# Performance work log

Hardware: AMD Instinct MI355X
Metric: run time of the kernel (lower is better)

Reference implementation:

```python
import jax, jax.numpy as jnp
import numpy as np

B, S, E, H, D, P = 4, 2048, 1024, 16, 64, 64  # batch, seq, embed, heads, head_dim, position_dim
MASKED_BIAS = -10000.0


def setup_inputs() -> dict:
    key = jax.random.key(0)
    ks = jax.random.split(key, 24)
    n = lambda k, sh: jax.random.normal(k, sh, dtype=jnp.float32)
    eyeD = jnp.eye(D, dtype=jnp.float32)
    eyeH = jnp.eye(H, dtype=jnp.float32)
    inp = {
        'hidden_states': n(ks[0], (B, S, E)),
        'position_states': n(ks[1], (B, S, P)),
        # Conv2D per-head projections (identity init + perturbation): [H, D, D]
        'Wq': eyeD[None] + 0.02 * n(ks[2], (H, D, D)), 'bq': 0.01 * n(ks[3], (H, D)),
        'Wk': eyeD[None] + 0.02 * n(ks[4], (H, D, D)), 'bk': 0.01 * n(ks[5], (H, D)),
        'Wv': eyeD[None] + 0.02 * n(ks[6], (H, D, D)), 'bv': 0.01 * n(ks[7], (H, D)),
        # Conv2D(transpose=True) cross-head mix: weight [H_out, H_in, D], bias [H, D]
        'Wqh': eyeH[:, :, None] + 0.02 * n(ks[8], (H, H, D)), 'bqh': 0.01 * n(ks[9], (H, D)),
        'Wkh': eyeH[:, :, None] + 0.02 * n(ks[10], (H, H, D)), 'bkh': 0.01 * n(ks[11], (H, D)),
        'Wvh': eyeH[:, :, None] + 0.02 * n(ks[12], (H, H, D)), 'bvh': 0.01 * n(ks[13], (H, D)),
        # p_attn Conv1D: position_dim -> 3*head_dim
        'Wp': 0.02 * n(ks[14], (P, 3 * D)), 'bp': 0.01 * n(ks[15], (3 * D,)),
        # position_conv expand: weight [3, 1, H], bias [H]
        'Wpe': 0.02 * n(ks[16], (3, 1, H)), 'bpe': 0.01 * n(ks[17], (H,)),
        # c_proj Conv1D: E -> E
        'Wc': 0.02 * n(ks[18], (E, E)), 'bc': 0.01 * n(ks[19], (E,)),
    }
    return inp


def _attention(hidden_states, position_states, Wq, bq, Wqh, bqh, Wk, bk, Wkh, bkh,
               Wv, bv, Wvh, bvh, Wp, bp, Wpe, bpe, Wc, bc):
    b, s, _ = hidden_states.shape
    x = hidden_states.reshape(b, s, H, D)

    def proj(Wa, ba, Wh, bh):
        # Conv2D: per-head linear within head_dim
        y = jnp.einsum('bshd,hde->bshe', x, Wa) + ba
        # Conv2D(transpose): mix across heads, per feature dim d
        return jnp.einsum('bshd,ghd->bsgd', y, Wh) + bh

    q = proj(Wq, bq, Wqh, bqh)  # [b,s,H,D]
    k = proj(Wk, bk, Wkh, bkh)
    v = proj(Wv, bv, Wvh, bvh)

    # p_attn (Conv1D) -> [b,s,3,D]; p_expand broadcasts each var across heads
    p = (position_states @ Wp + bp).reshape(b, s, 3, D)
    pe = p[..., None, :] * Wpe[:, 0, :][:, :, None] + bpe[:, None]  # [b,s,3,H,D]
    q = q + pe[:, :, 0]
    k = k + pe[:, :, 1]
    v = v + pe[:, :, 2]

    q = q.transpose(0, 2, 1, 3)  # [b,H,s,D]
    k = k.transpose(0, 2, 1, 3)
    v = v.transpose(0, 2, 1, 3)

    scores = jnp.einsum('bhqd,bhkd->bhqk', q, k) / jnp.sqrt(jnp.float32(D))
    causal = jnp.tril(jnp.ones((s, s), dtype=bool))
    scores = jnp.where(causal, scores, jnp.float32(MASKED_BIAS))
    w = jax.nn.softmax(scores, axis=-1)
    o = jnp.einsum('bhqk,bhkd->bhqd', w, v)
    o = o.transpose(0, 2, 1, 3).reshape(b, s, E)
    return o @ Wc + bc


def reference(hidden_states, position_states, Wq, bq, Wqh, bqh, Wk, bk, Wkh, bkh,
              Wv, bv, Wvh, bvh, Wp, bp, Wpe, bpe, Wc, bc):
    return _attention(hidden_states, position_states, Wq, bq, Wqh, bqh, Wk, bk,
                      Wkh, bkh, Wv, bv, Wvh, bvh, Wp, bp, Wpe, bpe, Wc, bc)
```

## Files before the change

kernel.cpp:

```cpp
#include <hip/hip_runtime.h>
#include <stdint.h>
#include <stddef.h>

using bf16x8 = __attribute__((ext_vector_type(8))) __bf16;
using f32x4  = __attribute__((ext_vector_type(4))) float;
using u16x8  = __attribute__((ext_vector_type(8))) unsigned short;
using u16x4  = __attribute__((ext_vector_type(4))) unsigned short;
typedef unsigned short u16;

#define DEV __device__ __forceinline__

#define QSCALE 0.18033688011112042f
#define SBIAS 32.0f

DEV u16 f2bf(float f) {
  unsigned u = __float_as_uint(f);
  u += 0x7fffu + ((u >> 16) & 1u);
  return (u16)(u >> 16);
}

DEV void gld_lds16(const u16* g, u16* l) {
  __builtin_amdgcn_global_load_lds(
      (__attribute__((address_space(1))) void*)g,
      (__attribute__((address_space(3))) void*)l, 16, 0, 0);
}

__global__ __launch_bounds__(256) void k_packA(const float* __restrict__ hs,
                                               const float* __restrict__ ps,
                                               u16* __restrict__ A) {
  int idx = blockIdx.x * 256 + threadIdx.x;
  int t  = idx / 272;
  int c4 = (idx - t * 272) * 4;
  float4 f;
  if (c4 < 1024) f = *(const float4*)(hs + (size_t)t * 1024 + c4);
  else           f = *(const float4*)(ps + (size_t)t * 64 + (c4 - 1024));
  u16x4 o4;
  o4[0] = f2bf(f.x); o4[1] = f2bf(f.y); o4[2] = f2bf(f.z); o4[3] = f2bf(f.w);
  *(u16x4*)(A + (size_t)t * 1088 + c4) = o4;
}

__global__ __launch_bounds__(256) void k_buildW(const float* __restrict__ Wq, const float* __restrict__ Wk,
                                                const float* __restrict__ Wv, const float* __restrict__ Wqh,
                                                const float* __restrict__ Wkh, const float* __restrict__ Wvh,
                                                const float* __restrict__ Wp, const float* __restrict__ Wpe,
                                                u16* __restrict__ Wt) {
  int idx = blockIdx.x * 256 + threadIdx.x;
  int n = idx / 1088, kk = idx - n * 1088;
  int which = n >> 10, g = (n >> 6) & 15, e = n & 63;
  const float* Wa = (which == 0) ? Wq : (which == 1) ? Wk : Wv;
  const float* Wh = (which == 0) ? Wqh : (which == 1) ? Wkh : Wvh;
  float val;
  if (kk < 1024) {
    int h = kk >> 6, d = kk & 63;
    val = Wa[(size_t)(h * 64 + d) * 64 + e] * Wh[(size_t)(g * 16 + h) * 64 + e];
  } else {
    int p = kk - 1024;
    val = Wp[(size_t)p * 192 + which * 64 + e] * Wpe[which * 16 + g];
  }
  if (which == 0) val *= QSCALE;
  Wt[idx] = f2bf(val);
}

__global__ __launch_bounds__(256) void k_buildBias(const float* __restrict__ bq, const float* __restrict__ bk,
                                                   const float* __restrict__ bv, const float* __restrict__ Wqh,
                                                   const float* __restrict__ Wkh, const float* __restrict__ Wvh,
                                                   const float* __restrict__ bqh, const float* __restrict__ bkh,
                                                   const float* __restrict__ bvh, const float* __restrict__ bp,
                                                   const float* __restrict__ Wpe, const float* __restrict__ bpe,
                                                   float* __restrict__ bias) {
  int n = blockIdx.x * 256 + threadIdx.x;
  int which = n >> 10, g = (n >> 6) & 15, e = n & 63;
  const float* ba = (which == 0) ? bq : (which == 1) ? bk : bv;
  const float* Wh = (which == 0) ? Wqh : (which == 1) ? Wkh : Wvh;
  const float* bh = (which == 0) ? bqh : (which == 1) ? bkh : bvh;
  float s = bh[g * 64 + e] + bp[which * 64 + e] * Wpe[which * 16 + g] + bpe[g];
  for (int h = 0; h < 16; ++h) s += ba[h * 64 + e] * Wh[(g * 16 + h) * 64 + e];
  if (which == 0) s *= QSCALE;
  bias[n] = s;
}

__global__ __launch_bounds__(256) void k_transWc(const float* __restrict__ Wc, u16* __restrict__ WcT) {
  __shared__ float tile[32][33];
  int tx = threadIdx.x & 31, ty = threadIdx.x >> 5;
  int n0 = blockIdx.x * 32, k0 = blockIdx.y * 32;
#pragma unroll
  for (int i = 0; i < 32; i += 8)
    tile[ty + i][tx] = Wc[(size_t)(k0 + ty + i) * 1024 + n0 + tx];
  __syncthreads();
#pragma unroll
  for (int i = 0; i < 32; i += 8)
    WcT[(size_t)(n0 + ty + i) * 1024 + k0 + tx] = f2bf(tile[tx][ty + i]);
}

template <int EPI>
__global__ __launch_bounds__(256) void gemm128(const u16* __restrict__ A, const u16* __restrict__ Bt,
                                               const float* __restrict__ bias,
                                               u16* __restrict__ qo, u16* __restrict__ ko, u16* __restrict__ vo,
                                               float* __restrict__ outf, int M, int N, int K, int NT) {
  __shared__ alignas(16) u16 As[2][8192];
  __shared__ alignas(16) u16 Bs[2][8192];
  const int tid = threadIdx.x;
  const int l = tid & 63, w = tid >> 6;
  const int lr = l & 15, lg = l >> 4;
  const int wm = w >> 1, wn = w & 1;

  const int nwg = gridDim.x;
  const int cpx = nwg >> 3;
  const int virt = (blockIdx.x & 7) * cpx + (blockIdx.x >> 3);
  const int m0 = (virt / NT) * 128, n0 = (virt - (virt / NT) * NT) * 128;

  const int KT = K >> 6;

  f32x4 acc[4][4] = {};

#pragma unroll
  for (int call = 0; call < 4; ++call) {
    int ci = (call * 4 + w) * 64 + l;
    int row = ci >> 3, s = ci & 7;
    int kq = (s ^ (row & 7)) * 8;
    gld_lds16(A + (size_t)(m0 + row) * K + kq, &As[0][(call * 4 + w) * 512]);
    gld_lds16(Bt + (size_t)(n0 + row) * K + kq, &Bs[0][(call * 4 + w) * 512]);
  }

  int cur = 0;
  for (int kt = 0; kt < KT; ++kt) {
    if (kt + 1 < KT) {
      const int kb = (kt + 1) * 64;
#pragma unroll
      for (int call = 0; call < 4; ++call) {
        int ci = (call * 4 + w) * 64 + l;
        int row = ci >> 3, s = ci & 7;
        int kq = (s ^ (row & 7)) * 8;
        gld_lds16(A + (size_t)(m0 + row) * K + kb + kq, &As[cur ^ 1][(call * 4 + w) * 512]);
        gld_lds16(Bt + (size_t)(n0 + row) * K + kb + kq, &Bs[cur ^ 1][(call * 4 + w) * 512]);
      }
      asm volatile("s_waitcnt vmcnt(8)" ::: "memory");
    } else {
      asm volatile("s_waitcnt vmcnt(0)" ::: "memory");
    }
    __builtin_amdgcn_s_barrier();
    asm volatile("" ::: "memory");

    const u16* AsC = As[cur];
    const u16* BsC = Bs[cur];
#pragma unroll
    for (int kk = 0; kk < 2; ++kk) {
      bf16x8 af[4], bfr[4];
#pragma unroll
      for (int mf = 0; mf < 4; ++mf) {
        int row = wm * 64 + mf * 16 + lr;
        int byo = row * 128 + (((kk * 32 + lg * 8) * 2) ^ ((row & 7) << 4));
        af[mf] = *(const bf16x8*)((const char*)AsC + byo);
      }
#pragma unroll
      for (int nf = 0; nf < 4; ++nf) {
        int row = wn * 64 + nf * 16 + lr;
        int byo = row * 128 + (((kk * 32 + lg * 8) * 2) ^ ((row & 7) << 4));
        bfr[nf] = *(const bf16x8*)((const char*)BsC + byo);
      }
      __builtin_amdgcn_s_setprio(1);
#pragma unroll
      for (int mf = 0; mf < 4; ++mf)
#pragma unroll
        for (int nf = 0; nf < 4; ++nf)
          acc[mf][nf] = __builtin_amdgcn_mfma_f32_16x16x32_bf16(af[mf], bfr[nf], acc[mf][nf], 0, 0, 0);
      __builtin_amdgcn_s_setprio(0);
    }

    asm volatile("s_waitcnt lgkmcnt(0)" ::: "memory");
    __builtin_amdgcn_s_barrier();
    asm volatile("" ::: "memory");
    cur ^= 1;
  }

#pragma unroll
  for (int mf = 0; mf < 4; ++mf)
#pragma unroll
    for (int nf = 0; nf < 4; ++nf)
#pragma unroll
      for (int r = 0; r < 4; ++r) {
        int row = m0 + wm * 64 + mf * 16 + lg * 4 + r;
        int col = n0 + wn * 64 + nf * 16 + lr;
        float val = acc[mf][nf][r] + bias[col];
        if (EPI == 0) {
          int which = col >> 10, g = (col >> 6) & 15, e = col & 63;
          int b = row >> 11, si = row & 2047;
          size_t idx = ((size_t)((b * 16 + g) * 2048 + si)) * 64 + e;
          u16 bvv = f2bf(val);
          if (which == 0) qo[idx] = bvv;
          else if (which == 1) ko[idx] = bvv;
          else vo[idx] = bvv;
        } else {
          outf[(size_t)row * N + col] = val;
        }
      }
}

__global__ __launch_bounds__(256) void k_transV(const u16* __restrict__ v, u16* __restrict__ vT) {
  __shared__ u16 t[64][65];
  int bh = blockIdx.y, s0 = blockIdx.x * 64;
  const u16* src = v + ((size_t)bh * 2048 + s0) * 64;
  u16* dst = vT + (size_t)bh * 64 * 2048 + s0;
  int tid = threadIdx.x;
#pragma unroll
  for (int it = 0; it < 2; ++it) {
    int ci = it * 256 + tid;
    int row = ci >> 3, sl = ci & 7;
    u16x8 val = *(const u16x8*)(src + (size_t)row * 64 + sl * 8);
#pragma unroll
    for (int jj = 0; jj < 8; ++jj) t[row][sl * 8 + jj] = val[jj];
  }
  __syncthreads();
#pragma unroll
  for (int it = 0; it < 2; ++it) {
    int ci = it * 256 + tid;
    int d = ci >> 3, sl = ci & 7;
    u16x8 val;
#pragma unroll
    for (int jj = 0; jj < 8; ++jj) {
      int cp = sl * 8 + jj;
      int tt = (cp & 3) * 16 + (cp >> 2);
      val[jj] = t[tt][d];
    }
    *(u16x8*)(dst + (size_t)d * 2048 + sl * 8) = val;
  }
}

__global__ __launch_bounds__(256) void k_attn(const u16* __restrict__ q, const u16* __restrict__ k,
                                              const u16* __restrict__ vt, u16* __restrict__ o) {
  __shared__ alignas(16) u16 Ks[2][4096];
  __shared__ alignas(16) u16 Vs[2][4096];
  __shared__ alignas(16) u16 Ps[4][32 * 72];

  const int tid = threadIdx.x, l = tid & 63, w = tid >> 6;
  const int lr = l & 15, lg = l >> 4;
  const int i = blockIdx.x;
  const int bh = (i & 7) * 8 + ((i >> 3) & 7);
  const int xb = i >> 6;
  const int b = bh >> 4, h = bh & 15;

  const u16* qp = q + (size_t)bh * 2048 * 64;
  const u16* kp = k + (size_t)bh * 2048 * 64;
  const u16* vp = vt + (size_t)bh * 64 * 2048;

  bf16x8 ones;
#pragma unroll
  for (int e = 0; e < 8; ++e) ones[e] = (__bf16)1.0f;

  for (int half = 0; half < 2; ++half) {
    const int tile = half ? (15 - xb) : xb;
    const int qr0 = tile * 128 + w * 32;
    const int jmax = 2 * tile + 1;
    const int jmask = (qr0 + 31) >> 6;

    bf16x8 qf[2][2];
#pragma unroll
    for (int mf = 0; mf < 2; ++mf)
#pragma unroll
      for (int kk = 0; kk < 2; ++kk)
        qf[mf][kk] = *(const bf16x8*)(qp + (size_t)(qr0 + mf * 16 + lr) * 64 + kk * 32 + lg * 8);

    f32x4 oacc[2][4] = {};
    f32x4 osum[2] = {};

#pragma unroll
    for (int c = 0; c < 2; ++c) {
      int ci = c * 256 + tid;
      int row = ci >> 3, s = ci & 7;
      int kq = (s ^ (row & 7)) * 8;
      gld_lds16(kp + (size_t)row * 64 + kq, &Ks[0][(c * 4 + w) * 512]);
      gld_lds16(vp + (size_t)row * 2048 + kq, &Vs[0][(c * 4 + w) * 512]);
    }

    int cur = 0;
    for (int j = 0; j <= jmax; ++j) {
      if (j < jmax) {
        const int jn = j + 1;
#pragma unroll
        for (int c = 0; c < 2; ++c) {
          int ci = c * 256 + tid;
          int row = ci >> 3, s = ci & 7;
          int kq = (s ^ (row & 7)) * 8;
          gld_lds16(kp + (size_t)(jn * 64 + row) * 64 + kq, &Ks[cur ^ 1][(c * 4 + w) * 512]);
          gld_lds16(vp + (size_t)row * 2048 + jn * 64 + kq, &Vs[cur ^ 1][(c * 4 + w) * 512]);
        }
        asm volatile("s_waitcnt vmcnt(4)" ::: "memory");
      } else {
        asm volatile("s_waitcnt vmcnt(0)" ::: "memory");
      }
      __builtin_amdgcn_s_barrier();
      asm volatile("" ::: "memory");

      if (j <= jmask) {
        const u16* KsC = Ks[cur];
        const u16* VsC = Vs[cur];

        f32x4 sfr[2][4];
#pragma unroll
        for (int mf = 0; mf < 2; ++mf)
#pragma unroll
          for (int nf = 0; nf < 4; ++nf)
            sfr[mf][nf] = f32x4{-SBIAS, -SBIAS, -SBIAS, -SBIAS};
#pragma unroll
        for (int kk = 0; kk < 2; ++kk) {
          bf16x8 bk[4];
#pragma unroll
          for (int nf = 0; nf < 4; ++nf) {
            int row = nf * 16 + lr;
            int byo = row * 128 + (((kk * 32 + lg * 8) * 2) ^ ((row & 7) << 4));
            bk[nf] = *(const bf16x8*)((const char*)KsC + byo);
          }
          __builtin_amdgcn_s_setprio(1);
#pragma unroll
          for (int mf = 0; mf < 2; ++mf)
#pragma unroll
            for (int nf = 0; nf < 4; ++nf)
              sfr[mf][nf] = __builtin_amdgcn_mfma_f32_16x16x32_bf16(qf[mf][kk], bk[nf], sfr[mf][nf], 0, 0, 0);
          __builtin_amdgcn_s_setprio(0);
        }

        const bool maskt = (j == jmask);
#pragma unroll
        for (int mf = 0; mf < 2; ++mf)
#pragma unroll
          for (int r = 0; r < 4; ++r) {
            float s0 = sfr[mf][0][r], s1 = sfr[mf][1][r], s2 = sfr[mf][2][r], s3 = sfr[mf][3][r];
            if (maskt) {
              int rowg = qr0 + mf * 16 + lg * 4 + r;
              int base = j * 64 + lr;
              if (base      > rowg) s0 = -1e30f;
              if (base + 16 > rowg) s1 = -1e30f;
              if (base + 32 > rowg) s2 = -1e30f;
              if (base + 48 > rowg) s3 = -1e30f;
            }
            float p0 = __builtin_amdgcn_exp2f(s0);
            float p1 = __builtin_amdgcn_exp2f(s1);
            float p2 = __builtin_amdgcn_exp2f(s2);
            float p3 = __builtin_amdgcn_exp2f(s3);
            unsigned w0, w1;
            asm("v_cvt_pk_bf16_f32 %0, %1, %2" : "=v"(w0) : "v"(p0), "v"(p1));
            asm("v_cvt_pk_bf16_f32 %0, %1, %2" : "=v"(w1) : "v"(p2), "v"(p3));
            uint2 pw; pw.x = w0; pw.y = w1;
            *(uint2*)&Ps[w][(mf * 16 + lg * 4 + r) * 72 + 4 * lr] = pw;
          }

#pragma unroll
        for (int kk = 0; kk < 2; ++kk) {
          bf16x8 pa[2];
#pragma unroll
          for (int mf = 0; mf < 2; ++mf)
            pa[mf] = *(const bf16x8*)&Ps[w][(mf * 16 + lr) * 72 + kk * 32 + lg * 8];
          bf16x8 bv[4];
#pragma unroll
          for (int df = 0; df < 4; ++df) {
            int row = df * 16 + lr;
            int byo = row * 128 + (((kk * 32 + lg * 8) * 2) ^ ((row & 7) << 4));
            bv[df] = *(const bf16x8*)((const char*)VsC + byo);
          }
          __builtin_amdgcn_s_setprio(1);
#pragma unroll
          for (int mf = 0; mf < 2; ++mf)
#pragma unroll
            for (int df = 0; df < 4; ++df)
              oacc[mf][df] = __builtin_amdgcn_mfma_f32_16x16x32_bf16(pa[mf], bv[df], oacc[mf][df], 0, 0, 0);
#pragma unroll
          for (int mf = 0; mf < 2; ++mf)
            osum[mf] = __builtin_amdgcn_mfma_f32_16x16x32_bf16(pa[mf], ones, osum[mf], 0, 0, 0);
          __builtin_amdgcn_s_setprio(0);
        }
      }

      asm volatile("s_waitcnt lgkmcnt(0)" ::: "memory");
      __builtin_amdgcn_s_barrier();
      asm volatile("" ::: "memory");
      cur ^= 1;
    }

#pragma unroll
    for (int mf = 0; mf < 2; ++mf)
#pragma unroll
      for (int r = 0; r < 4; ++r) {
        float inv = 1.0f / osum[mf][r];
        int rowg = qr0 + mf * 16 + lg * 4 + r;
#pragma unroll
        for (int df = 0; df < 4; ++df)
          o[((size_t)(b * 2048 + rowg)) * 1024 + h * 64 + df * 16 + lr] = f2bf(oacc[mf][df][r] * inv);
      }
  }
}

extern "C" void kernel_launch(void* const* d_in, const int* in_sizes, int n_in,
                              void* d_out, int out_size, void* d_ws, size_t ws_size,
                              hipStream_t stream) {
  const float* hs  = (const float*)d_in[0];
  const float* pos = (const float*)d_in[1];
  const float* Wq  = (const float*)d_in[2];  const float* bq  = (const float*)d_in[3];
  const float* Wk  = (const float*)d_in[4];  const float* bk  = (const float*)d_in[5];
  const float* Wv  = (const float*)d_in[6];  const float* bv  = (const float*)d_in[7];
  const float* Wqh = (const float*)d_in[8];  const float* bqh = (const float*)d_in[9];
  const float* Wkh = (const float*)d_in[10]; const float* bkh = (const float*)d_in[11];
  const float* Wvh = (const float*)d_in[12]; const float* bvh = (const float*)d_in[13];
  const float* Wp  = (const float*)d_in[14]; const float* bp  = (const float*)d_in[15];
  const float* Wpe = (const float*)d_in[16]; const float* bpe = (const float*)d_in[17];
  const float* Wc  = (const float*)d_in[18]; const float* bc  = (const float*)d_in[19];
  float* out = (float*)d_out;
  char* ws = (char*)d_ws;

  u16*   Abf   = (u16*)  (ws + 0);
  u16*   WT    = (u16*)  (ws + 17825792);
  float* biasq = (float*)(ws + 24510464);
  u16*   WcT   = (u16*)  (ws + 24522752);
  u16*   qb_   = (u16*)  (ws + 26619904);
  u16*   kb_   = (u16*)  (ws + 43397120);
  u16*   vb_   = (u16*)  (ws + 60174336);
  u16*   vTb   = (u16*)  (ws + 76951552);
  u16*   ob    = Abf;

  k_packA<<<8704, 256, 0, stream>>>(hs, pos, Abf);
  k_buildW<<<13056, 256, 0, stream>>>(Wq, Wk, Wv, Wqh, Wkh, Wvh, Wp, Wpe, WT);
  k_buildBias<<<12, 256, 0, stream>>>(bq, bk, bv, Wqh, Wkh, Wvh, bqh, bkh, bvh, bp, Wpe, bpe, biasq);
  k_transWc<<<dim3(32, 32), 256, 0, stream>>>(Wc, WcT);
  gemm128<0><<<1536, 256, 0, stream>>>(Abf, WT, biasq, qb_, kb_, vb_, nullptr, 8192, 3072, 1088, 24);
  k_transV<<<dim3(32, 64), 256, 0, stream>>>(vb_, vTb);
  k_attn<<<512, 256, 0, stream>>>(qb_, kb_, vTb, ob);
  gemm128<1><<<512, 256, 0, stream>>>(ob, WcT, bc, nullptr, nullptr, nullptr, out, 8192, 1024, 1024, 8);
}
```

Baseline: 188.0 us.

## Use 256-row query tiles with 8-wave attention blocks and fuse prep kernels

The attention kernel now runs 512-thread blocks of 8 waves, each covering a 256-row query tile. Each staged K/V chunk is therefore shared by twice as many query rows, which cuts global K/V loads and lets each thread issue a single async load per chunk. The causal tile pairing is updated to match: 8 tiles per sequence, paired as xb and 7-xb. Separately, the four weight and input preparation kernels are merged into one launch that dispatches on block index, removing three launch overheads. The risk is coarser scheduling and possibly lower occupancy from the larger blocks.

```diff
diff --git a/kernel.cpp b/kernel.cpp
--- a/kernel.cpp
+++ b/kernel.cpp
@@ -25,71 +25,68 @@
       (__attribute__((address_space(3))) void*)l, 16, 0, 0);
 }
 
-__global__ __launch_bounds__(256) void k_packA(const float* __restrict__ hs,
-                                               const float* __restrict__ ps,
-                                               u16* __restrict__ A) {
-  int idx = blockIdx.x * 256 + threadIdx.x;
-  int t  = idx / 272;
-  int c4 = (idx - t * 272) * 4;
-  float4 f;
-  if (c4 < 1024) f = *(const float4*)(hs + (size_t)t * 1024 + c4);
-  else           f = *(const float4*)(ps + (size_t)t * 64 + (c4 - 1024));
-  u16x4 o4;
-  o4[0] = f2bf(f.x); o4[1] = f2bf(f.y); o4[2] = f2bf(f.z); o4[3] = f2bf(f.w);
-  *(u16x4*)(A + (size_t)t * 1088 + c4) = o4;
-}
-
-__global__ __launch_bounds__(256) void k_buildW(const float* __restrict__ Wq, const float* __restrict__ Wk,
-                                                const float* __restrict__ Wv, const float* __restrict__ Wqh,
-                                                const float* __restrict__ Wkh, const float* __restrict__ Wvh,
-                                                const float* __restrict__ Wp, const float* __restrict__ Wpe,
-                                                u16* __restrict__ Wt) {
-  int idx = blockIdx.x * 256 + threadIdx.x;
-  int n = idx / 1088, kk = idx - n * 1088;
-  int which = n >> 10, g = (n >> 6) & 15, e = n & 63;
-  const float* Wa = (which == 0) ? Wq : (which == 1) ? Wk : Wv;
-  const float* Wh = (which == 0) ? Wqh : (which == 1) ? Wkh : Wvh;
-  float val;
-  if (kk < 1024) {
-    int h = kk >> 6, d = kk & 63;
-    val = Wa[(size_t)(h * 64 + d) * 64 + e] * Wh[(size_t)(g * 16 + h) * 64 + e];
+__global__ __launch_bounds__(256) void k_prep(const float* __restrict__ hs, const float* __restrict__ ps,
+                                              const float* __restrict__ Wq, const float* __restrict__ Wk,
+                                              const float* __restrict__ Wv, const float* __restrict__ Wqh,
+                                              const float* __restrict__ Wkh, const float* __restrict__ Wvh,
+                                              const float* __restrict__ Wp, const float* __restrict__ Wpe,
+                                              const float* __restrict__ bq, const float* __restrict__ bk,
+                                              const float* __restrict__ bv, const float* __restrict__ bqh,
+                                              const float* __restrict__ bkh, const float* __restrict__ bvh,
+                                              const float* __restrict__ bp, const float* __restrict__ bpe,
+                                              const float* __restrict__ Wc,
+                                              u16* __restrict__ A, u16* __restrict__ Wt,
+                                              float* __restrict__ bias, u16* __restrict__ WcT) {
+  const int bid = blockIdx.x;
+  if (bid < 8704) {
+    int idx = bid * 256 + threadIdx.x;
+    int t  = idx / 272;
+    int c4 = (idx - t * 272) * 4;
+    float4 f;
+    if (c4 < 1024) f = *(const float4*)(hs + (size_t)t * 1024 + c4);
+    else           f = *(const float4*)(ps + (size_t)t * 64 + (c4 - 1024));
+    u16x4 o4;
+    o4[0] = f2bf(f.x); o4[1] = f2bf(f.y); o4[2] = f2bf(f.z); o4[3] = f2bf(f.w);
+    *(u16x4*)(A + (size_t)t * 1088 + c4) = o4;
+  } else if (bid < 21760) {
+    int idx = (bid - 8704) * 256 + threadIdx.x;
+    int n = idx / 1088, kk = idx - n * 1088;
+    int which = n >> 10, g = (n >> 6) & 15, e = n & 63;
+    const float* Wa = (which == 0) ? Wq : (which == 1) ? Wk : Wv;
+    const float* Wh = (which == 0) ? Wqh : (which == 1) ? Wkh : Wvh;
+    float val;
+    if (kk < 1024) {
+      int h = kk >> 6, d = kk & 63;
+      val = Wa[(size_t)(h * 64 + d) * 64 + e] * Wh[(size_t)(g * 16 + h) * 64 + e];
+    } else {
+      int p = kk - 1024;
+      val = Wp[(size_t)p * 192 + which * 64 + e] * Wpe[which * 16 + g];
+    }
+    if (which == 0) val *= QSCALE;
+    Wt[idx] = f2bf(val);
+  } else if (bid < 21772) {
+    int n = (bid - 21760) * 256 + threadIdx.x;
+    int which = n >> 10, g = (n >> 6) & 15, e = n & 63;
+    const float* ba = (which == 0) ? bq : (which == 1) ? bk : bv;
+    const float* Wh = (which == 0) ? Wqh : (which == 1) ? Wkh : Wvh;
+    const float* bh = (which == 0) ? bqh : (which == 1) ? bkh : bvh;
+    float s = bh[g * 64 + e] + bp[which * 64 + e] * Wpe[which * 16 + g] + bpe[g];
+    for (int h = 0; h < 16; ++h) s += ba[h * 64 + e] * Wh[(g * 16 + h) * 64 + e];
+    if (which == 0) s *= QSCALE;
+    bias[n] = s;
   } else {
-    int p = kk - 1024;
-    val = Wp[(size_t)p * 192 + which * 64 + e] * Wpe[which * 16 + g];
-  }
-  if (which == 0) val *= QSCALE;
-  Wt[idx] = f2bf(val);
-}
-
-__global__ __launch_bounds__(256) void k_buildBias(const float* __restrict__ bq, const float* __restrict__ bk,
-                                                   const float* __restrict__ bv, const float* __restrict__ Wqh,
-                                                   const float* __restrict__ Wkh, const float* __restrict__ Wvh,
-                                                   const float* __restrict__ bqh, const float* __restrict__ bkh,
-                                                   const float* __restrict__ bvh, const float* __restrict__ bp,
-                                                   const float* __restrict__ Wpe, const float* __restrict__ bpe,
-                                                   float* __restrict__ bias) {
-  int n = blockIdx.x * 256 + threadIdx.x;
-  int which = n >> 10, g = (n >> 6) & 15, e = n & 63;
-  const float* ba = (which == 0) ? bq : (which == 1) ? bk : bv;
-  const float* Wh = (which == 0) ? Wqh : (which == 1) ? Wkh : Wvh;
-  const float* bh = (which == 0) ? bqh : (which == 1) ? bkh : bvh;
-  float s = bh[g * 64 + e] + bp[which * 64 + e] * Wpe[which * 16 + g] + bpe[g];
-  for (int h = 0; h < 16; ++h) s += ba[h * 64 + e] * Wh[(g * 16 + h) * 64 + e];
-  if (which == 0) s *= QSCALE;
-  bias[n] = s;
-}
-
-__global__ __launch_bounds__(256) void k_transWc(const float* __restrict__ Wc, u16* __restrict__ WcT) {
-  __shared__ float tile[32][33];
-  int tx = threadIdx.x & 31, ty = threadIdx.x >> 5;
-  int n0 = blockIdx.x * 32, k0 = blockIdx.y * 32;
-#pragma unroll
-  for (int i = 0; i < 32; i += 8)
-    tile[ty + i][tx] = Wc[(size_t)(k0 + ty + i) * 1024 + n0 + tx];
-  __syncthreads();
-#pragma unroll
-  for (int i = 0; i < 32; i += 8)
-    WcT[(size_t)(n0 + ty + i) * 1024 + k0 + tx] = f2bf(tile[tx][ty + i]);
+    __shared__ float tile[32][33];
+    int t = bid - 21772;
+    int tx = threadIdx.x & 31, ty = threadIdx.x >> 5;
+    int n0 = (t & 31) * 32, k0 = (t >> 5) * 32;
+#pragma unroll
+    for (int i = 0; i < 32; i += 8)
+      tile[ty + i][tx] = Wc[(size_t)(k0 + ty + i) * 1024 + n0 + tx];
+    __syncthreads();
+#pragma unroll
+    for (int i = 0; i < 32; i += 8)
+      WcT[(size_t)(n0 + ty + i) * 1024 + k0 + tx] = f2bf(tile[tx][ty + i]);
+  }
 }
 
 template <int EPI>
@@ -226,11 +223,11 @@
   }
 }
 
-__global__ __launch_bounds__(256) void k_attn(const u16* __restrict__ q, const u16* __restrict__ k,
+__global__ __launch_bounds__(512) void k_attn(const u16* __restrict__ q, const u16* __restrict__ k,
                                               const u16* __restrict__ vt, u16* __restrict__ o) {
   __shared__ alignas(16) u16 Ks[2][4096];
   __shared__ alignas(16) u16 Vs[2][4096];
-  __shared__ alignas(16) u16 Ps[4][32 * 72];
+  __shared__ alignas(16) u16 Ps[8][32 * 72];
 
   const int tid = threadIdx.x, l = tid & 63, w = tid >> 6;
   const int lr = l & 15, lg = l >> 4;
@@ -243,15 +240,18 @@
   const u16* kp = k + (size_t)bh * 2048 * 64;
   const u16* vp = vt + (size_t)bh * 64 * 2048;
 
+  const int srow = tid >> 3;
+  const int skq = ((tid & 7) ^ (srow & 7)) * 8;
+
   bf16x8 ones;
 #pragma unroll
   for (int e = 0; e < 8; ++e) ones[e] = (__bf16)1.0f;
 
   for (int half = 0; half < 2; ++half) {
-    const int tile = half ? (15 - xb) : xb;
-    const int qr0 = tile * 128 + w * 32;
-    const int jmax = 2 * tile + 1;
-    const int jmask = (qr0 + 31) >> 6;
+    const int tile = half ? (7 - xb) : xb;
+    const int qr0 = tile * 256 + w * 32;
+    const int jmax = 4 * tile + 3;
+    const int jmask = qr0 >> 6;
 
     bf16x8 qf[2][2];
 #pragma unroll
@@ -263,28 +263,16 @@
     f32x4 oacc[2][4] = {};
     f32x4 osum[2] = {};
 
-#pragma unroll
-    for (int c = 0; c < 2; ++c) {
-      int ci = c * 256 + tid;
-      int row = ci >> 3, s = ci & 7;
-      int kq = (s ^ (row & 7)) * 8;
-      gld_lds16(kp + (size_t)row * 64 + kq, &Ks[0][(c * 4 + w) * 512]);
-      gld_lds16(vp + (size_t)row * 2048 + kq, &Vs[0][(c * 4 + w) * 512]);
-    }
+    gld_lds16(kp + (size_t)srow * 64 + skq, &Ks[0][w * 512]);
+    gld_lds16(vp + (size_t)srow * 2048 + skq, &Vs[0][w * 512]);
 
     int cur = 0;
     for (int j = 0; j <= jmax; ++j) {
       if (j < jmax) {
         const int jn = j + 1;
-#pragma unroll
-        for (int c = 0; c < 2; ++c) {
-          int ci = c * 256 + tid;
-          int row = ci >> 3, s = ci & 7;
-          int kq = (s ^ (row & 7)) * 8;
-          gld_lds16(kp + (size_t)(jn * 64 + row) * 64 + kq, &Ks[cur ^ 1][(c * 4 + w) * 512]);
-          gld_lds16(vp + (size_t)row * 2048 + jn * 64 + kq, &Vs[cur ^ 1][(c * 4 + w) * 512]);
-        }
-        asm volatile("s_waitcnt vmcnt(4)" ::: "memory");
+        gld_lds16(kp + (size_t)(jn * 64 + srow) * 64 + skq, &Ks[cur ^ 1][w * 512]);
+        gld_lds16(vp + (size_t)srow * 2048 + jn * 64 + skq, &Vs[cur ^ 1][w * 512]);
+        asm volatile("s_waitcnt vmcnt(2)" ::: "memory");
       } else {
         asm volatile("s_waitcnt vmcnt(0)" ::: "memory");
       }
@@ -416,12 +404,11 @@
   u16*   vTb   = (u16*)  (ws + 76951552);
   u16*   ob    = Abf;
 
-  k_packA<<<8704, 256, 0, stream>>>(hs, pos, Abf);
-  k_buildW<<<13056, 256, 0, stream>>>(Wq, Wk, Wv, Wqh, Wkh, Wvh, Wp, Wpe, WT);
-  k_buildBias<<<12, 256, 0, stream>>>(bq, bk, bv, Wqh, Wkh, Wvh, bqh, bkh, bvh, bp, Wpe, bpe, biasq);
-  k_transWc<<<dim3(32, 32), 256, 0, stream>>>(Wc, WcT);
+  k_prep<<<22796, 256, 0, stream>>>(hs, pos, Wq, Wk, Wv, Wqh, Wkh, Wvh, Wp, Wpe,
+                                    bq, bk, bv, bqh, bkh, bvh, bp, bpe, Wc,
+                                    Abf, WT, biasq, WcT);
   gemm128<0><<<1536, 256, 0, stream>>>(Abf, WT, biasq, qb_, kb_, vb_, nullptr, 8192, 3072, 1088, 24);
   k_transV<<<dim3(32, 64), 256, 0, stream>>>(vb_, vTb);
-  k_attn<<<512, 256, 0, stream>>>(qb_, kb_, vTb, ob);
+  k_attn<<<512, 512, 0, stream>>>(qb_, kb_, vTb, ob);
   gemm128<1><<<512, 256, 0, stream>>>(ob, WcT, bc, nullptr, nullptr, nullptr, out, 8192, 1024, 1024, 8);
 }
```

Result: slower. 239.5 us (+27.4%).
